# Kernel optimization log

Measured on AMD Instinct MI355X. Metric: run time of the kernel, lower is better.

## Reference

```python
import jax, jax.numpy as jnp
import numpy as np

N_HEAD = 16

def setup_inputs() -> dict:
    key = jax.random.key(0)
    ks = jax.random.split(key, 5)
    B, T, D = 2, 2048, 1024
    k = D // N_HEAD
    scale = 0.02
    return {
        'x': jax.random.normal(ks[0], (B, T, D), dtype=jnp.float32),
        'Wq': jax.random.normal(ks[1], (D, D), dtype=jnp.float32) * scale,
        'Wk': jax.random.normal(ks[2], (D, k), dtype=jnp.float32) * scale,
        'Wv': jax.random.normal(ks[3], (D, k), dtype=jnp.float32) * scale,
        'Wo': jax.random.normal(ks[4], (D, D), dtype=jnp.float32) * scale,
    }

def reference(x, Wq, Wk, Wv, Wo):
    B, T, D = x.shape
    h = N_HEAD
    k = D // h
    Q = (x @ Wq).reshape(B, T, h, k)          # per-head queries
    K = x @ Wk                                 # single shared K head: (B,T,k)
    V = x @ Wv                                 # single shared V head: (B,T,k)
    scores = jnp.einsum('bthk,bsk->bhts', Q, K) / jnp.sqrt(jnp.float32(k))
    causal = jnp.tril(jnp.ones((T, T), dtype=bool))  # (T,T)
    scores = jnp.where(causal[None, None, :, :], scores, -jnp.inf)
    A = jax.nn.softmax(scores, axis=-1)        # (B,h,T,T)
    Y = jnp.einsum('bhts,bsk->bthk', A, V).reshape(B, T, D)
    return Y @ Wo
```

## Files before the change

kernel.cpp:

```cpp
#include <hip/hip_runtime.h>
#include <hip/hip_bf16.h>
#include <stdint.h>

typedef short short8 __attribute__((ext_vector_type(8)));
typedef float f32x4 __attribute__((ext_vector_type(4)));

constexpr int SEQ   = 2048;
constexpr int DM    = 1024;
constexpr int NHEAD = 16;
constexpr int HD    = 64;
constexpr int LDQ   = 1152;
constexpr int BATCH = 2;

__device__ __forceinline__ unsigned short f2bf(float f) {
    union { float f; uint32_t u; } v; v.f = f;
    uint32_t u = v.u;
    uint32_t r = (u + 0x7fffu + ((u >> 16) & 1u)) >> 16;
    return (unsigned short)r;
}

typedef __attribute__((address_space(1))) const void gvoid_t;
typedef __attribute__((address_space(3))) void lvoid_t;
__device__ __forceinline__ void gload16(const void* g, void* l) {
    __builtin_amdgcn_global_load_lds((gvoid_t*)g, (lvoid_t*)l, 16, 0, 0);
}

__global__ __launch_bounds__(256) void cast_x_kernel(
        const float* __restrict__ x, unsigned short* __restrict__ xb, int n) {
    int i = (blockIdx.x * 256 + threadIdx.x) * 4;
    if (i >= n) return;
    const float4 v = *(const float4*)(x + i);
    ushort4 o;
    o.x = f2bf(v.x); o.y = f2bf(v.y); o.z = f2bf(v.z); o.w = f2bf(v.w);
    *(ushort4*)(xb + i) = o;
}

__global__ __launch_bounds__(256) void prep_w_kernel(
        const float* __restrict__ Wq, const float* __restrict__ Wk,
        const float* __restrict__ Wv, const float* __restrict__ Wo,
        unsigned short* __restrict__ wtq, unsigned short* __restrict__ wot) {
    __shared__ unsigned short tile[32][33];
    int z = blockIdx.z;
    const float* W; unsigned short* Wt; int C;
    if (z == 0)      { W = Wq; Wt = wtq;                              C = DM; }
    else if (z == 1) { W = Wk; Wt = wtq + (size_t)DM * DM;            C = HD; }
    else if (z == 2) { W = Wv; Wt = wtq + (size_t)(DM + HD) * DM;     C = HD; }
    else             { W = Wo; Wt = wot;                              C = DM; }
    int c0 = blockIdx.x * 32, r0 = blockIdx.y * 32;
    if (c0 >= C) return;
    int tx = threadIdx.x & 31, ty = threadIdx.x >> 5;
    for (int i = ty; i < 32; i += 8)
        tile[i][tx] = f2bf(W[(size_t)(r0 + i) * C + (c0 + tx)]);
    __syncthreads();
    for (int i = ty; i < 32; i += 8)
        Wt[(size_t)(c0 + i) * DM + (r0 + tx)] = tile[tx][i];
}

__global__ __launch_bounds__(256) void gemm_kernel(
        const unsigned short* __restrict__ A,
        const unsigned short* __restrict__ Bt,
        void* __restrict__ Cout,
        unsigned short* __restrict__ VtOut,
        int M, int N, int K, int out_bf16, int ncols) {
    __shared__ unsigned short ldsA[2][128 * 64];
    __shared__ unsigned short ldsB[2][64 * 64];
    int lane = threadIdx.x & 63, wave = threadIdx.x >> 6;
    int ln = lane & 15, quad = lane >> 4;
    int wm = wave >> 1, wn = wave & 1;

    int g = blockIdx.x;
    int xcd = g & 7, idx = g >> 3;
    int rows_per_xcd = (int)(gridDim.x >> 3) / ncols;
    int row = xcd * rows_per_xcd + idx / ncols;
    int col = idx % ncols;
    int m0 = row * 128, n0 = col * 64;

    int t = threadIdx.x;
    int trow = t >> 3, tcb = t & 7;
    int gcb = tcb ^ (trow & 7);
    const unsigned short* gA = A + (size_t)(m0 + trow) * K + gcb * 8;
    const unsigned short* gB = Bt + (size_t)(n0 + trow) * K + gcb * 8;
    int dst = t * 8;

    auto stage = [&](int k0, int buf) {
#pragma unroll
        for (int rr = 0; rr < 4; ++rr)
            gload16(gA + (size_t)rr * 32 * K + k0, &ldsA[buf][dst + rr * 2048]);
#pragma unroll
        for (int rr = 0; rr < 2; ++rr)
            gload16(gB + (size_t)rr * 32 * K + k0, &ldsB[buf][dst + rr * 2048]);
    };

    f32x4 acc[4][2];
#pragma unroll
    for (int i = 0; i < 4; ++i)
#pragma unroll
        for (int j = 0; j < 2; ++j) acc[i][j] = f32x4{0, 0, 0, 0};

    stage(0, 0);
    int niter = K >> 6;
    for (int it = 0; it < niter; ++it) {
        __syncthreads();
        if (it + 1 < niter) stage((it + 1) << 6, (it + 1) & 1);
        const unsigned short* La = ldsA[it & 1];
        const unsigned short* Lb = ldsB[it & 1];
#pragma unroll
        for (int hh = 0; hh < 2; ++hh) {
            int kc = hh * 4 + quad;
            short8 aF[4], bF[2];
#pragma unroll
            for (int mt = 0; mt < 4; ++mt)
                aF[mt] = *(const short8*)&La[(wm * 64 + mt * 16 + ln) * 64 +
                                             ((kc ^ (ln & 7)) * 8)];
#pragma unroll
            for (int nt = 0; nt < 2; ++nt)
                bF[nt] = *(const short8*)&Lb[(wn * 32 + nt * 16 + ln) * 64 +
                                             ((kc ^ (ln & 7)) * 8)];
#pragma unroll
            for (int mt = 0; mt < 4; ++mt)
#pragma unroll
                for (int nt = 0; nt < 2; ++nt)
                    acc[mt][nt] = __builtin_amdgcn_mfma_f32_16x16x32_bf16(
                        aF[mt], bF[nt], acc[mt][nt], 0, 0, 0);
        }
    }

    if (out_bf16) {
        unsigned short* C = (unsigned short*)Cout;
#pragma unroll
        for (int mt = 0; mt < 4; ++mt)
#pragma unroll
            for (int nt = 0; nt < 2; ++nt)
#pragma unroll
                for (int r = 0; r < 4; ++r) {
                    int rr = m0 + wm * 64 + mt * 16 + quad * 4 + r;
                    int cc = n0 + wn * 32 + nt * 16 + ln;
                    unsigned short hv = f2bf(acc[mt][nt][r]);
                    C[(size_t)rr * N + cc] = hv;
                    if (VtOut != nullptr && cc >= DM + HD) {
                        int d = cc - (DM + HD);
                        int bb = rr >> 11, s = rr & 2047;
                        VtOut[((size_t)bb * HD + d) * SEQ + s] = hv;
                    }
                }
    } else {
        float* C = (float*)Cout;
#pragma unroll
        for (int mt = 0; mt < 4; ++mt)
#pragma unroll
            for (int nt = 0; nt < 2; ++nt)
#pragma unroll
                for (int r = 0; r < 4; ++r) {
                    int rr = m0 + wm * 64 + mt * 16 + quad * 4 + r;
                    int cc = n0 + wn * 32 + nt * 16 + ln;
                    C[(size_t)rr * N + cc] = acc[mt][nt][r];
                }
    }
}

__global__ __launch_bounds__(512) void attn_kernel(
        const unsigned short* __restrict__ QKV,
        const unsigned short* __restrict__ Vt,
        unsigned short* __restrict__ Y) {
    __shared__ unsigned short ldsK[2][64 * 64];
    __shared__ unsigned short ldsV[2][64 * 64];
    __shared__ unsigned short pbuf[8][16 * 64];

    int lane = threadIdx.x & 63, wave = threadIdx.x >> 6;
    int ln = lane & 15, quad = lane >> 4;
    int bid = blockIdx.x;
    int jg = 15 - (bid >> 5);
    int bh = bid & 31;
    int h = bh & 15, b = bh >> 4;
    int q0 = (jg * 8 + wave) * 16;
    const size_t baseRow = (size_t)b * SEQ;
    const unsigned short* Vb = Vt + (size_t)b * HD * SEQ;

    int t = threadIdx.x;
    int trow = t >> 3, tcb = t & 7;
    int cbg = tcb ^ (trow & 7);
    const unsigned short* gK = QKV + (baseRow + trow) * LDQ + DM + cbg * 8;
    const unsigned short* gV = Vb + (size_t)trow * SEQ + cbg * 8;
    int dstoff = t * 8;

    auto stageKV = [&](int s0n, int buf) {
        gload16(gK + (size_t)s0n * LDQ, &ldsK[buf][dstoff]);
        gload16(gV + s0n,               &ldsV[buf][dstoff]);
    };

    short8 aQ0, aQ1;
    {
        const unsigned short* qp = QKV + (baseRow + q0 + ln) * LDQ + h * HD + quad * 8;
        aQ0 = *(const short8*)(qp);
        aQ1 = *(const short8*)(qp + 32);
    }

    float lsum[4] = {0.f, 0.f, 0.f, 0.f};
    f32x4 o[4];
    for (int nt = 0; nt < 4; ++nt) o[nt] = f32x4{0, 0, 0, 0};

    const float c_exp = 0.1803368802f;
    unsigned short* pb = &pbuf[wave][0];

    auto computeStep = [&](int s0, int buf, bool partial) {
        const unsigned short* Kb = ldsK[buf];
        const unsigned short* Vf = ldsV[buf];
#pragma unroll
        for (int c = 0; c < 4; ++c) {
            int kbase = s0 + c * 16;
            if (partial && kbase > q0 + 15) {
#pragma unroll
                for (int r = 0; r < 4; ++r) {
                    int row = quad * 4 + r;
                    pb[row * 64 + (((c * 2 + (ln >> 3)) ^ (row & 7)) * 8) + (ln & 7)] = 0;
                }
                continue;
            }
            short8 k0f = *(const short8*)&Kb[(c * 16 + ln) * 64 + ((quad ^ (ln & 7)) * 8)];
            short8 k1f = *(const short8*)&Kb[(c * 16 + ln) * 64 + (((4 + quad) ^ (ln & 7)) * 8)];
            f32x4 s = {0, 0, 0, 0};
            s = __builtin_amdgcn_mfma_f32_16x16x32_bf16(aQ0, k0f, s, 0, 0, 0);
            s = __builtin_amdgcn_mfma_f32_16x16x32_bf16(aQ1, k1f, s, 0, 0, 0);
            bool diag = partial && (kbase + 15 > q0);
#pragma unroll
            for (int r = 0; r < 4; ++r) {
                float e = __builtin_exp2f(s[r] * c_exp);
                if (diag && (kbase + ln > q0 + quad * 4 + r)) e = 0.f;
                lsum[r] += e;
                int row = quad * 4 + r;
                pb[row * 64 + (((c * 2 + (ln >> 3)) ^ (row & 7)) * 8) + (ln & 7)] =
                    (unsigned short)(__float_as_uint(e) >> 16);
            }
        }
        short8 aP0 = *(const short8*)&pb[ln * 64 + ((quad ^ (ln & 7)) * 8)];
        short8 aP1 = *(const short8*)&pb[ln * 64 + (((4 + quad) ^ (ln & 7)) * 8)];
#pragma unroll
        for (int nt = 0; nt < 4; ++nt) {
            short8 v0 = *(const short8*)&Vf[(nt * 16 + ln) * 64 + ((quad ^ (ln & 7)) * 8)];
            short8 v1 = *(const short8*)&Vf[(nt * 16 + ln) * 64 + (((4 + quad) ^ (ln & 7)) * 8)];
            o[nt] = __builtin_amdgcn_mfma_f32_16x16x32_bf16(aP0, v0, o[nt], 0, 0, 0);
            o[nt] = __builtin_amdgcn_mfma_f32_16x16x32_bf16(aP1, v1, o[nt], 0, 0, 0);
        }
    };

    int nfull  = 2 * jg + (wave >> 2);
    int nsteps = 2 * jg + 2;
    stageKV(0, 0);
    for (int it = 0; it < nsteps; ++it) {
        __syncthreads();
        if (it + 1 < nsteps) stageKV((it + 1) * 64, (it + 1) & 1);
        if (it < nfull)       computeStep(it * 64, it & 1, false);
        else if (it == nfull) computeStep(it * 64, it & 1, true);
    }

    for (int off = 1; off < 16; off <<= 1)
#pragma unroll
        for (int r = 0; r < 4; ++r) lsum[r] += __shfl_xor(lsum[r], off);
#pragma unroll
    for (int r = 0; r < 4; ++r) {
        float inv = 1.0f / lsum[r];
        int t_idx = q0 + quad * 4 + r;
        unsigned short* yp = Y + (baseRow + t_idx) * DM + h * HD + ln;
        for (int nt = 0; nt < 4; ++nt)
            yp[nt * 16] = f2bf(o[nt][r] * inv);
    }
}

extern "C" void kernel_launch(void* const* d_in, const int* in_sizes, int n_in,
                              void* d_out, int out_size, void* d_ws, size_t ws_size,
                              hipStream_t stream) {
    const float* x  = (const float*)d_in[0];
    const float* Wq = (const float*)d_in[1];
    const float* Wk = (const float*)d_in[2];
    const float* Wv = (const float*)d_in[3];
    const float* Wo = (const float*)d_in[4];
    float* out = (float*)d_out;

    char* ws = (char*)d_ws;
    unsigned short* xb  = (unsigned short*)(ws);
    unsigned short* y   = (unsigned short*)(ws);
    unsigned short* wtq = (unsigned short*)(ws + 8388608);
    unsigned short* wot = (unsigned short*)(ws + 10747904);
    unsigned short* qkv = (unsigned short*)(ws + 12845056);
    unsigned short* Vt  = (unsigned short*)(ws + 22282240);

    const int BT = BATCH * SEQ;

    hipLaunchKernelGGL(cast_x_kernel, dim3(BT * DM / 4 / 256), dim3(256), 0, stream,
                       x, xb, BT * DM);
    hipLaunchKernelGGL(prep_w_kernel, dim3(DM / 32, DM / 32, 4), dim3(256), 0, stream,
                       Wq, Wk, Wv, Wo, wtq, wot);

    hipLaunchKernelGGL(gemm_kernel, dim3((BT / 128) * (LDQ / 64)), dim3(256), 0, stream,
                       xb, wtq, (void*)qkv, Vt, BT, LDQ, DM, 1, LDQ / 64);

    hipLaunchKernelGGL(attn_kernel, dim3(16 * 32), dim3(512), 0, stream,
                       qkv, Vt, y);

    hipLaunchKernelGGL(gemm_kernel, dim3((BT / 128) * (DM / 64)), dim3(256), 0, stream,
                       y, wot, (void*)out, nullptr, BT, DM, DM, 0, DM / 64);
}
```

Before: 169.2 us.

## Triple-buffer GEMM LDS pipeline and shrink attention blocks to four waves

The GEMM now keeps three LDS stages with loads issued two iterations ahead. It waits with an explicit vmcnt count and a raw barrier instead of __syncthreads, so global latency overlaps more compute. The attention kernel now uses 256-thread blocks covering 64 query rows, with twice as many blocks. Every wave in a block shares the same diagonal step, which removes the idle-wave imbalance of the 8-wave layout and improves load spread across CUs. The GEMM uses more LDS, and the manual waitcnt depends on the exact number of loads issued per stage.

```diff
diff --git a/kernel.cpp b/kernel.cpp
--- a/kernel.cpp
+++ b/kernel.cpp
@@ -62,8 +62,8 @@
         void* __restrict__ Cout,
         unsigned short* __restrict__ VtOut,
         int M, int N, int K, int out_bf16, int ncols) {
-    __shared__ unsigned short ldsA[2][128 * 64];
-    __shared__ unsigned short ldsB[2][64 * 64];
+    __shared__ unsigned short ldsA[3][128 * 64];
+    __shared__ unsigned short ldsB[3][64 * 64];
     int lane = threadIdx.x & 63, wave = threadIdx.x >> 6;
     int ln = lane & 15, quad = lane >> 4;
     int wm = wave >> 1, wn = wave & 1;
@@ -97,13 +97,19 @@
 #pragma unroll
         for (int j = 0; j < 2; ++j) acc[i][j] = f32x4{0, 0, 0, 0};
 
+    int niter = K >> 6;
     stage(0, 0);
-    int niter = K >> 6;
+    stage(64, 1);
     for (int it = 0; it < niter; ++it) {
-        __syncthreads();
-        if (it + 1 < niter) stage((it + 1) << 6, (it + 1) & 1);
-        const unsigned short* La = ldsA[it & 1];
-        const unsigned short* Lb = ldsB[it & 1];
+        if (it + 1 < niter)
+            asm volatile("s_waitcnt vmcnt(6)" ::: "memory");
+        else
+            asm volatile("s_waitcnt vmcnt(0)" ::: "memory");
+        __builtin_amdgcn_s_barrier();
+        __builtin_amdgcn_sched_barrier(0);
+        if (it + 2 < niter) stage((it + 2) << 6, (it + 2) % 3);
+        const unsigned short* La = ldsA[it % 3];
+        const unsigned short* Lb = ldsB[it % 3];
 #pragma unroll
         for (int hh = 0; hh < 2; ++hh) {
             int kc = hh * 4 + quad;
@@ -158,21 +164,21 @@
     }
 }
 
-__global__ __launch_bounds__(512) void attn_kernel(
+__global__ __launch_bounds__(256) void attn_kernel(
         const unsigned short* __restrict__ QKV,
         const unsigned short* __restrict__ Vt,
         unsigned short* __restrict__ Y) {
     __shared__ unsigned short ldsK[2][64 * 64];
     __shared__ unsigned short ldsV[2][64 * 64];
-    __shared__ unsigned short pbuf[8][16 * 64];
+    __shared__ unsigned short pbuf[4][16 * 64];
 
     int lane = threadIdx.x & 63, wave = threadIdx.x >> 6;
     int ln = lane & 15, quad = lane >> 4;
     int bid = blockIdx.x;
-    int jg = 15 - (bid >> 5);
+    int jg = 31 - (bid >> 5);
     int bh = bid & 31;
     int h = bh & 15, b = bh >> 4;
-    int q0 = (jg * 8 + wave) * 16;
+    int q0 = (jg * 4 + wave) * 16;
     const size_t baseRow = (size_t)b * SEQ;
     const unsigned short* Vb = Vt + (size_t)b * HD * SEQ;
 
@@ -181,11 +187,14 @@
     int cbg = tcb ^ (trow & 7);
     const unsigned short* gK = QKV + (baseRow + trow) * LDQ + DM + cbg * 8;
     const unsigned short* gV = Vb + (size_t)trow * SEQ + cbg * 8;
-    int dstoff = t * 8;
+    int dstoff = trow * 64 + tcb * 8;
 
     auto stageKV = [&](int s0n, int buf) {
-        gload16(gK + (size_t)s0n * LDQ, &ldsK[buf][dstoff]);
-        gload16(gV + s0n,               &ldsV[buf][dstoff]);
+#pragma unroll
+        for (int rr = 0; rr < 2; ++rr) {
+            gload16(gK + (size_t)(s0n + 32 * rr) * LDQ, &ldsK[buf][dstoff + rr * 2048]);
+            gload16(gV + (size_t)32 * rr * SEQ + s0n,   &ldsV[buf][dstoff + rr * 2048]);
+        }
     };
 
     short8 aQ0, aQ1;
@@ -243,15 +252,14 @@
         }
     };
 
-    int nfull  = 2 * jg + (wave >> 2);
-    int nsteps = 2 * jg + 2;
     stageKV(0, 0);
-    for (int it = 0; it < nsteps; ++it) {
+    for (int it = 0; it < jg; ++it) {
         __syncthreads();
-        if (it + 1 < nsteps) stageKV((it + 1) * 64, (it + 1) & 1);
-        if (it < nfull)       computeStep(it * 64, it & 1, false);
-        else if (it == nfull) computeStep(it * 64, it & 1, true);
-    }
+        stageKV((it + 1) * 64, (it + 1) & 1);
+        computeStep(it * 64, it & 1, false);
+    }
+    __syncthreads();
+    computeStep(jg * 64, jg & 1, true);
 
     for (int off = 1; off < 16; off <<= 1)
 #pragma unroll
@@ -294,7 +302,7 @@
     hipLaunchKernelGGL(gemm_kernel, dim3((BT / 128) * (LDQ / 64)), dim3(256), 0, stream,
                        xb, wtq, (void*)qkv, Vt, BT, LDQ, DM, 1, LDQ / 64);
 
-    hipLaunchKernelGGL(attn_kernel, dim3(16 * 32), dim3(512), 0, stream,
+    hipLaunchKernelGGL(attn_kernel, dim3(32 * 32), dim3(256), 0, stream,
                        qkv, Vt, y);
 
     hipLaunchKernelGGL(gemm_kernel, dim3((BT / 128) * (DM / 64)), dim3(256), 0, stream,
```

Measured after the change: 175.0 us. +3.4%, slower.

## Process two 16-row query tiles per wave in attention to reuse K/V fragments

Applied to the files above, without the earlier changes.

Each wave of the attention kernel now handles 32 query rows as two 16-row sub-tiles, so every K and V fragment read from LDS feeds two MFMAs. Blocks shrink from 8 waves to 4, and each thread stages two rows of the K/V tiles. Block-to-query-group ordering is interleaved to balance causal work across the grid. The cost is more accumulator registers per thread and fewer waves per block to hide latency.

```diff
diff --git a/kernel.cpp b/kernel.cpp
--- a/kernel.cpp
+++ b/kernel.cpp
@@ -158,21 +158,23 @@
     }
 }
 
-__global__ __launch_bounds__(512) void attn_kernel(
+__global__ __launch_bounds__(256) void attn_kernel(
         const unsigned short* __restrict__ QKV,
         const unsigned short* __restrict__ Vt,
         unsigned short* __restrict__ Y) {
     __shared__ unsigned short ldsK[2][64 * 64];
     __shared__ unsigned short ldsV[2][64 * 64];
-    __shared__ unsigned short pbuf[8][16 * 64];
+    __shared__ unsigned short pbuf[4][32 * 64];
 
     int lane = threadIdx.x & 63, wave = threadIdx.x >> 6;
     int ln = lane & 15, quad = lane >> 4;
     int bid = blockIdx.x;
-    int jg = 15 - (bid >> 5);
+    int gq = bid >> 5;
+    int jg = (gq < 8) ? (15 - 2 * gq) : (2 * (gq - 8));
     int bh = bid & 31;
     int h = bh & 15, b = bh >> 4;
-    int q0 = (jg * 8 + wave) * 16;
+    int w2 = jg * 4 + wave;
+    int q0 = w2 * 32;
     const size_t baseRow = (size_t)b * SEQ;
     const unsigned short* Vb = Vt + (size_t)b * HD * SEQ;
 
@@ -181,23 +183,34 @@
     int cbg = tcb ^ (trow & 7);
     const unsigned short* gK = QKV + (baseRow + trow) * LDQ + DM + cbg * 8;
     const unsigned short* gV = Vb + (size_t)trow * SEQ + cbg * 8;
-    int dstoff = t * 8;
+    int dstoff = trow * 64 + tcb * 8;
 
     auto stageKV = [&](int s0n, int buf) {
-        gload16(gK + (size_t)s0n * LDQ, &ldsK[buf][dstoff]);
-        gload16(gV + s0n,               &ldsV[buf][dstoff]);
+#pragma unroll
+        for (int rr = 0; rr < 2; ++rr) {
+            gload16(gK + (size_t)(s0n + 32 * rr) * LDQ, &ldsK[buf][dstoff + rr * 2048]);
+            gload16(gV + (size_t)32 * rr * SEQ + s0n,   &ldsV[buf][dstoff + rr * 2048]);
+        }
     };
 
-    short8 aQ0, aQ1;
-    {
-        const unsigned short* qp = QKV + (baseRow + q0 + ln) * LDQ + h * HD + quad * 8;
-        aQ0 = *(const short8*)(qp);
-        aQ1 = *(const short8*)(qp + 32);
+    short8 aQ[2][2];
+#pragma unroll
+    for (int u = 0; u < 2; ++u) {
+        const unsigned short* qp =
+            QKV + (baseRow + q0 + u * 16 + ln) * LDQ + h * HD + quad * 8;
+        aQ[u][0] = *(const short8*)(qp);
+        aQ[u][1] = *(const short8*)(qp + 32);
     }
 
-    float lsum[4] = {0.f, 0.f, 0.f, 0.f};
-    f32x4 o[4];
-    for (int nt = 0; nt < 4; ++nt) o[nt] = f32x4{0, 0, 0, 0};
+    float lsum[2][4];
+    f32x4 o[2][4];
+#pragma unroll
+    for (int u = 0; u < 2; ++u)
+#pragma unroll
+        for (int nt = 0; nt < 4; ++nt) {
+            o[u][nt] = f32x4{0, 0, 0, 0};
+            lsum[u][nt] = 0.f;
+        }
 
     const float c_exp = 0.1803368802f;
     unsigned short* pb = &pbuf[wave][0];
@@ -208,42 +221,63 @@
 #pragma unroll
         for (int c = 0; c < 4; ++c) {
             int kbase = s0 + c * 16;
-            if (partial && kbase > q0 + 15) {
-#pragma unroll
-                for (int r = 0; r < 4; ++r) {
-                    int row = quad * 4 + r;
-                    pb[row * 64 + (((c * 2 + (ln >> 3)) ^ (row & 7)) * 8) + (ln & 7)] = 0;
-                }
+            if (partial && kbase > q0 + 31) {
+#pragma unroll
+                for (int u = 0; u < 2; ++u)
+#pragma unroll
+                    for (int r = 0; r < 4; ++r) {
+                        int row = u * 16 + quad * 4 + r;
+                        pb[row * 64 + (((c * 2 + (ln >> 3)) ^ (row & 7)) * 8) + (ln & 7)] = 0;
+                    }
                 continue;
             }
             short8 k0f = *(const short8*)&Kb[(c * 16 + ln) * 64 + ((quad ^ (ln & 7)) * 8)];
             short8 k1f = *(const short8*)&Kb[(c * 16 + ln) * 64 + (((4 + quad) ^ (ln & 7)) * 8)];
-            f32x4 s = {0, 0, 0, 0};
-            s = __builtin_amdgcn_mfma_f32_16x16x32_bf16(aQ0, k0f, s, 0, 0, 0);
-            s = __builtin_amdgcn_mfma_f32_16x16x32_bf16(aQ1, k1f, s, 0, 0, 0);
-            bool diag = partial && (kbase + 15 > q0);
-#pragma unroll
-            for (int r = 0; r < 4; ++r) {
-                float e = __builtin_exp2f(s[r] * c_exp);
-                if (diag && (kbase + ln > q0 + quad * 4 + r)) e = 0.f;
-                lsum[r] += e;
-                int row = quad * 4 + r;
-                pb[row * 64 + (((c * 2 + (ln >> 3)) ^ (row & 7)) * 8) + (ln & 7)] =
-                    (unsigned short)(__float_as_uint(e) >> 16);
+#pragma unroll
+            for (int u = 0; u < 2; ++u) {
+                int q0u = q0 + u * 16;
+                if (partial && kbase > q0u + 15) {
+#pragma unroll
+                    for (int r = 0; r < 4; ++r) {
+                        int row = u * 16 + quad * 4 + r;
+                        pb[row * 64 + (((c * 2 + (ln >> 3)) ^ (row & 7)) * 8) + (ln & 7)] = 0;
+                    }
+                    continue;
+                }
+                f32x4 s2 = {0, 0, 0, 0};
+                s2 = __builtin_amdgcn_mfma_f32_16x16x32_bf16(aQ[u][0], k0f, s2, 0, 0, 0);
+                s2 = __builtin_amdgcn_mfma_f32_16x16x32_bf16(aQ[u][1], k1f, s2, 0, 0, 0);
+                bool diag = partial && (kbase + 15 > q0u);
+#pragma unroll
+                for (int r = 0; r < 4; ++r) {
+                    float e = __builtin_exp2f(s2[r] * c_exp);
+                    if (diag && (kbase + ln > q0u + quad * 4 + r)) e = 0.f;
+                    lsum[u][r] += e;
+                    int row = u * 16 + quad * 4 + r;
+                    pb[row * 64 + (((c * 2 + (ln >> 3)) ^ (row & 7)) * 8) + (ln & 7)] =
+                        (unsigned short)(__float_as_uint(e) >> 16);
+                }
             }
         }
-        short8 aP0 = *(const short8*)&pb[ln * 64 + ((quad ^ (ln & 7)) * 8)];
-        short8 aP1 = *(const short8*)&pb[ln * 64 + (((4 + quad) ^ (ln & 7)) * 8)];
+        short8 aP[2][2];
+#pragma unroll
+        for (int u = 0; u < 2; ++u) {
+            aP[u][0] = *(const short8*)&pb[(u * 16 + ln) * 64 + ((quad ^ (ln & 7)) * 8)];
+            aP[u][1] = *(const short8*)&pb[(u * 16 + ln) * 64 + (((4 + quad) ^ (ln & 7)) * 8)];
+        }
 #pragma unroll
         for (int nt = 0; nt < 4; ++nt) {
             short8 v0 = *(const short8*)&Vf[(nt * 16 + ln) * 64 + ((quad ^ (ln & 7)) * 8)];
             short8 v1 = *(const short8*)&Vf[(nt * 16 + ln) * 64 + (((4 + quad) ^ (ln & 7)) * 8)];
-            o[nt] = __builtin_amdgcn_mfma_f32_16x16x32_bf16(aP0, v0, o[nt], 0, 0, 0);
-            o[nt] = __builtin_amdgcn_mfma_f32_16x16x32_bf16(aP1, v1, o[nt], 0, 0, 0);
+#pragma unroll
+            for (int u = 0; u < 2; ++u) {
+                o[u][nt] = __builtin_amdgcn_mfma_f32_16x16x32_bf16(aP[u][0], v0, o[u][nt], 0, 0, 0);
+                o[u][nt] = __builtin_amdgcn_mfma_f32_16x16x32_bf16(aP[u][1], v1, o[u][nt], 0, 0, 0);
+            }
         }
     };
 
-    int nfull  = 2 * jg + (wave >> 2);
+    int nfull  = w2 >> 1;
     int nsteps = 2 * jg + 2;
     stageKV(0, 0);
     for (int it = 0; it < nsteps; ++it) {
@@ -255,15 +289,19 @@
 
     for (int off = 1; off < 16; off <<= 1)
 #pragma unroll
-        for (int r = 0; r < 4; ++r) lsum[r] += __shfl_xor(lsum[r], off);
-#pragma unroll
-    for (int r = 0; r < 4; ++r) {
-        float inv = 1.0f / lsum[r];
-        int t_idx = q0 + quad * 4 + r;
-        unsigned short* yp = Y + (baseRow + t_idx) * DM + h * HD + ln;
-        for (int nt = 0; nt < 4; ++nt)
-            yp[nt * 16] = f2bf(o[nt][r] * inv);
-    }
+        for (int u = 0; u < 2; ++u)
+#pragma unroll
+            for (int r = 0; r < 4; ++r) lsum[u][r] += __shfl_xor(lsum[u][r], off);
+#pragma unroll
+    for (int u = 0; u < 2; ++u)
+#pragma unroll
+        for (int r = 0; r < 4; ++r) {
+            float inv = 1.0f / lsum[u][r];
+            int t_idx = q0 + u * 16 + quad * 4 + r;
+            unsigned short* yp = Y + (baseRow + t_idx) * DM + h * HD + ln;
+            for (int nt = 0; nt < 4; ++nt)
+                yp[nt * 16] = f2bf(o[u][nt][r] * inv);
+        }
 }
 
 extern "C" void kernel_launch(void* const* d_in, const int* in_sizes, int n_in,
@@ -294,7 +332,7 @@
     hipLaunchKernelGGL(gemm_kernel, dim3((BT / 128) * (LDQ / 64)), dim3(256), 0, stream,
                        xb, wtq, (void*)qkv, Vt, BT, LDQ, DM, 1, LDQ / 64);
 
-    hipLaunchKernelGGL(attn_kernel, dim3(16 * 32), dim3(512), 0, stream,
+    hipLaunchKernelGGL(attn_kernel, dim3(16 * 32), dim3(256), 0, stream,
                        qkv, Vt, y);
 
     hipLaunchKernelGGL(gemm_kernel, dim3((BT / 128) * (DM / 64)), dim3(256), 0, stream,
```

New measurement: 183.8 us. 8.7% more time.
